# Optimization experiments

Hardware: AMD Instinct MI355X
Metric: run time of the kernel (lower is better)

Reference implementation:

```python
import jax, jax.numpy as jnp
import numpy as np

# dims
B, S, E, H, W = 32, 256, 512, 512, 512   # batch, max_sentence_length, word_emb, rnn_units, weight_size
ENC = 2 * H                               # bidirectional encoder hidden
V = 50000                                 # vocab


def setup_inputs() -> dict:
    key = jax.random.key(0)
    ks = jax.random.split(key, 16)
    n = jax.random.normal
    return {
        "word_ids": jax.random.randint(ks[0], (B, S), 0, V),
        "encoder_outputs": n(ks[1], (B, S, ENC), jnp.float32),
        "encoder_hn": n(ks[2], (B, H), jnp.float32),          # initial decoder cell state
        "emb": n(ks[3], (V, E), jnp.float32) * 0.02,          # WordFeature embedding table
        "chunk_emb": n(ks[4], (S, W), jnp.float32) * 0.02,    # chunk_length_embedding
        "W1": n(ks[5], (ENC, W), jnp.float32) / np.sqrt(ENC),
        "W2": n(ks[6], (E, W), jnp.float32) / np.sqrt(E),
        "W3": n(ks[7], (E, W), jnp.float32) / np.sqrt(E),
        "W4": n(ks[8], (H, W), jnp.float32) / np.sqrt(H),
        "vt1": n(ks[9], (W,), jnp.float32) / np.sqrt(W),
        "vt2": n(ks[10], (W,), jnp.float32) / np.sqrt(W),
        "Wx": n(ks[11], (E, 4 * H), jnp.float32) / np.sqrt(E),  # decoder LSTM cell
        "Wh": n(ks[12], (H, 4 * H), jnp.float32) / np.sqrt(H),
        "bias": jnp.zeros((4 * H,), jnp.float32),
    }


def reference(word_ids, encoder_outputs, encoder_hn, emb, chunk_emb,
              W1, W2, W3, W4, vt1, vt2, Wx, Wh, bias):
    Ss = word_ids.shape[1]
    Hh = encoder_hn.shape[1]
    inp = emb[word_ids]                                   # [B,S,E] word features
    b1 = jnp.einsum('bse,ew->bsw', encoder_outputs, W1)   # W1(encoder_output), hoisted
    b2 = jnp.einsum('bse,ew->bsw', inp, W2)               # W2(single_input), hoisted
    pos = jnp.arange(Ss)

    def decode_one(inp_b, b1_b, b2_b, c0):
        def step(carry, _):
            last_bond, bond, h, c, out_vec = carry
            done = bond >= Ss
            # decoder input: mean of current segment inp[last_bond:bond] (zeros at step 0)
            m = ((pos >= last_bond) & (pos < bond)).astype(inp_b.dtype)  # [S]
            x = (m @ inp_b) / jnp.maximum(m.sum(), 1.0)                  # [E]
            # LSTM cell (stand-in for decoder.pointer_forward)
            gates = x @ Wx + h @ Wh + bias                               # [4H]
            i_g, f_g, g_g, o_g = jnp.split(gates, 4)
            c_n = jax.nn.sigmoid(f_g) * c + jax.nn.sigmoid(i_g) * jnp.tanh(g_g)
            h_n = jax.nn.sigmoid(o_g) * jnp.tanh(c_n)
            h2 = jnp.where(done, h, h_n)
            c2 = jnp.where(done, c, c_n)
            bidx = jnp.minimum(bond, Ss - 1)
            # pointer attention over positions >= bond
            blend = jnp.tanh(b1_b + b2_b + inp_b[bidx] @ W3 + h2 @ W4)   # [S,W]
            seg_len = jnp.clip(bond - last_bond, 0, Ss - 1)
            scores = blend @ vt1 + chunk_emb[seg_len] @ vt2              # [S]
            scores = jnp.where(pos >= bidx, scores, -1e30)
            # log_softmax is monotonic -> argmax of scores == argmax of log-probs
            idx = jnp.argmax(scores)                                     # absolute = max_index + bond
            new_bond = jnp.where(idx > bond, idx, bond + 1)              # force progress
            widx = jnp.minimum(new_bond, Ss - 1)
            val = jnp.where((~done) & (new_bond < Ss), 1.0, out_vec[widx])
            out_new = out_vec.at[widx].set(val)
            last2 = jnp.where(done, last_bond, bond)
            bond2 = jnp.where(done, bond, new_bond)
            return (last2, bond2, h2, c2, out_new), None

        init = (jnp.int32(0), jnp.int32(0),
                jnp.zeros((Hh,), inp_b.dtype), c0,
                jnp.zeros((Ss,), inp_b.dtype))
        (_, _, _, _, out_vec), _ = jax.lax.scan(step, init, None, length=Ss)
        return out_vec

    outs = jax.vmap(decode_one)(inp, b1, b2, encoder_hn)   # [B,S]
    return outs.T                                          # [S,B] == torch.stack(output_list, 1)
```

## Files before the change

kernel.cpp:

```cpp
#include <hip/hip_runtime.h>
#include <math.h>

#define Bn   32
#define Sn   256
#define En   512
#define Hn   512
#define Wn   512
#define ENCn 1024
#define G4   2048
#define KTOT 1536

#define OFF_BSUM  0L
#define OFF_PWX   4194304L
#define OFF_PE    21037056L
#define OFF_U3    21037056L
#define OFF_WHB   25247744L
#define OFF_W4B   26296320L
#define OFF_GPH   26558464L
#define OFF_SPART 26689536L
#define OFF_STATE 26820608L

typedef unsigned long long u64t;

__device__ __forceinline__ float aload(const float* p) {
    return __hip_atomic_load(p, __ATOMIC_RELAXED, __HIP_MEMORY_SCOPE_AGENT);
}
__device__ __forceinline__ void astore(float* p, float v) {
    __hip_atomic_store(p, v, __ATOMIC_RELAXED, __HIP_MEMORY_SCOPE_AGENT);
}
__device__ __forceinline__ int aiload(const int* p) {
    return __hip_atomic_load(p, __ATOMIC_RELAXED, __HIP_MEMORY_SCOPE_AGENT);
}
__device__ __forceinline__ void aistore(int* p, int v) {
    __hip_atomic_store(p, v, __ATOMIC_RELAXED, __HIP_MEMORY_SCOPE_AGENT);
}
__device__ __forceinline__ u64t aload64(const u64t* p) {
    return __hip_atomic_load(p, __ATOMIC_RELAXED, __HIP_MEMORY_SCOPE_AGENT);
}
__device__ __forceinline__ void astore64(u64t* p, u64t v) {
    __hip_atomic_store(p, v, __ATOMIC_RELAXED, __HIP_MEMORY_SCOPE_AGENT);
}
__device__ __forceinline__ u64t pack2(float a, float b) {
    return (u64t)__float_as_uint(a) | ((u64t)__float_as_uint(b) << 32);
}
__device__ __forceinline__ float lo32(u64t v) { return __uint_as_float((unsigned)(v & 0xffffffffu)); }
__device__ __forceinline__ float hi32(u64t v) { return __uint_as_float((unsigned)(v >> 32)); }

__global__ void init_kernel(float* __restrict__ gph, int* __restrict__ state)
{
    int i = blockIdx.x * blockDim.x + threadIdx.x;
    if (i < 131072) gph[i] = 0.0f;
    if (i < 8192) state[i] = (i < 512) ? 1 : 0;
}

__global__ void wtrans_kernel(const float* __restrict__ Wh, const float* __restrict__ W4,
                              float* __restrict__ WhB, float* __restrict__ W4B)
{
    int idx = blockIdx.x * 256 + threadIdx.x;
    if (idx < 1048576) {
        const int c = idx & 255, k = (idx >> 8) & 511, cb = idx >> 17;
        WhB[idx] = Wh[(long)k * G4 + cb * 256 + c];
    }
    if (idx < 262144) {
        const int cc = idx & 3, l = (idx >> 2) & 63, kq = (idx >> 8) & 127, cb = idx >> 15;
        const int k = 4 * kq + cc, j = cb * 64 + l;
        W4B[idx] = W4[(long)k * Wn + j];
    }
}

__global__ void pe1_kernel(const int* __restrict__ wid, const float* __restrict__ emb,
                           float* __restrict__ pb)
{
    const int b = blockIdx.x, blk = blockIdx.y;
    __shared__ int wids[16];
    if (threadIdx.x < 16) wids[threadIdx.x] = wid[b * Sn + blk * 16 + threadIdx.x];
    __syncthreads();
    float a0 = 0.f, a1 = 0.f;
    for (int s = 0; s < 16; ++s) {
        const float* r = emb + (long)wids[s] * En;
        a0 += r[threadIdx.x]; a1 += r[threadIdx.x + 256];
    }
    pb[((long)b * 16 + blk) * En + threadIdx.x] = a0;
    pb[((long)b * 16 + blk) * En + threadIdx.x + 256] = a1;
}

__global__ void pe2_kernel(const int* __restrict__ wid, const float* __restrict__ emb,
                           const float* __restrict__ pb, float* __restrict__ pe)
{
    const int b = blockIdx.x, blk = blockIdx.y;
    __shared__ int wids[16];
    if (threadIdx.x < 16) wids[threadIdx.x] = wid[b * Sn + blk * 16 + threadIdx.x];
    __syncthreads();
    float a0 = 0.f, a1 = 0.f;
    for (int j = 0; j < blk; ++j) {
        a0 += pb[((long)b * 16 + j) * En + threadIdx.x];
        a1 += pb[((long)b * 16 + j) * En + threadIdx.x + 256];
    }
    float* base = pe + (long)b * 257 * En;
    if (blk == 0) { base[threadIdx.x] = 0.f; base[threadIdx.x + 256] = 0.f; }
    for (int s = 0; s < 16; ++s) {
        const float* r = emb + (long)wids[s] * En;
        a0 += r[threadIdx.x]; a1 += r[threadIdx.x + 256];
        float* o = base + (long)(blk * 16 + s + 1) * En;
        o[threadIdx.x] = a0; o[threadIdx.x + 256] = a1;
    }
}

__global__ __launch_bounds__(256) void bsum_gemm(
    const float* __restrict__ enc, const int* __restrict__ wid,
    const float* __restrict__ emb, const float* __restrict__ W1,
    const float* __restrict__ W2, float* __restrict__ bsum)
{
    __shared__ float As[16][68];
    __shared__ float Bs[16][68];
    const int tid  = threadIdx.x;
    const int row0 = blockIdx.y * 64;
    const int col0 = blockIdx.x * 64;
    const int tm0  = (tid & 15) * 4;
    const int tn0  = (tid >> 4) * 4;
    const int la_r = tid >> 2;
    const int la_k = (tid & 3) * 4;
    const int lb_k = tid >> 4;
    const int lb_n = (tid & 15) * 4;

    float acc[4][4];
#pragma unroll
    for (int i = 0; i < 4; i++)
#pragma unroll
        for (int j = 0; j < 4; j++) acc[i][j] = 0.0f;

    for (int k0 = 0; k0 < KTOT; k0 += 16) {
        const int gr = row0 + la_r;
        float4 av;
        if (k0 < ENCn) {
            av = *(const float4*)&enc[(long)gr * ENCn + k0 + la_k];
        } else {
            const int wv = wid[gr];
            av = *(const float4*)&emb[(long)wv * En + (k0 - ENCn) + la_k];
        }
        As[la_k + 0][la_r] = av.x;
        As[la_k + 1][la_r] = av.y;
        As[la_k + 2][la_r] = av.z;
        As[la_k + 3][la_r] = av.w;
        float4 bv;
        if (k0 < ENCn) bv = *(const float4*)&W1[(long)(k0 + lb_k) * Wn + col0 + lb_n];
        else           bv = *(const float4*)&W2[(long)(k0 - ENCn + lb_k) * Wn + col0 + lb_n];
        *(float4*)&Bs[lb_k][lb_n] = bv;
        __syncthreads();
#pragma unroll
        for (int kk = 0; kk < 16; kk++) {
            float4 a = *(const float4*)&As[kk][tm0];
            float4 b = *(const float4*)&Bs[kk][tn0];
            acc[0][0] += a.x * b.x; acc[0][1] += a.x * b.y; acc[0][2] += a.x * b.z; acc[0][3] += a.x * b.w;
            acc[1][0] += a.y * b.x; acc[1][1] += a.y * b.y; acc[1][2] += a.y * b.z; acc[1][3] += a.y * b.w;
            acc[2][0] += a.z * b.x; acc[2][1] += a.z * b.y; acc[2][2] += a.z * b.z; acc[2][3] += a.z * b.w;
            acc[3][0] += a.w * b.x; acc[3][1] += a.w * b.y; acc[3][2] += a.w * b.z; acc[3][3] += a.w * b.w;
        }
        __syncthreads();
    }
#pragma unroll
    for (int i = 0; i < 4; i++) {
        float4 o = make_float4(acc[i][0], acc[i][1], acc[i][2], acc[i][3]);
        *(float4*)&bsum[(long)(row0 + tm0 + i) * Wn + col0 + tn0] = o;
    }
}

__global__ __launch_bounds__(256) void swx_gemm(
    const float* __restrict__ pe, const float* __restrict__ Wx, float* __restrict__ PWX)
{
    __shared__ float As[16][68];
    __shared__ float Bs[16][68];
    const int tid  = threadIdx.x;
    const int row0 = blockIdx.y * 64;
    const int col0 = blockIdx.x * 64;
    const int tm0  = (tid & 15) * 4;
    const int tn0  = (tid >> 4) * 4;
    const int la_r = tid >> 2;
    const int la_k = (tid & 3) * 4;
    const int lb_k = tid >> 4;
    const int lb_n = (tid & 15) * 4;

    float acc[4][4];
#pragma unroll
    for (int i = 0; i < 4; i++)
#pragma unroll
        for (int j = 0; j < 4; j++) acc[i][j] = 0.0f;

    for (int k0 = 0; k0 < 512; k0 += 16) {
        int gr = row0 + la_r; if (gr > 8223) gr = 8223;
        float4 av = *(const float4*)&pe[(long)gr * En + k0 + la_k];
        As[la_k + 0][la_r] = av.x;
        As[la_k + 1][la_r] = av.y;
        As[la_k + 2][la_r] = av.z;
        As[la_k + 3][la_r] = av.w;
        *(float4*)&Bs[lb_k][lb_n] = *(const float4*)&Wx[(long)(k0 + lb_k) * G4 + col0 + lb_n];
        __syncthreads();
#pragma unroll
        for (int kk = 0; kk < 16; kk++) {
            float4 a = *(const float4*)&As[kk][tm0];
            float4 b = *(const float4*)&Bs[kk][tn0];
            acc[0][0] += a.x * b.x; acc[0][1] += a.x * b.y; acc[0][2] += a.x * b.z; acc[0][3] += a.x * b.w;
            acc[1][0] += a.y * b.x; acc[1][1] += a.y * b.y; acc[1][2] += a.y * b.z; acc[1][3] += a.y * b.w;
            acc[2][0] += a.z * b.x; acc[2][1] += a.z * b.y; acc[2][2] += a.z * b.z; acc[2][3] += a.z * b.w;
            acc[3][0] += a.w * b.x; acc[3][1] += a.w * b.y; acc[3][2] += a.w * b.z; acc[3][3] += a.w * b.w;
        }
        __syncthreads();
    }
#pragma unroll
    for (int i = 0; i < 4; i++) {
        const int r = row0 + tm0 + i;
        if (r < 8224) {
            float4 o = make_float4(acc[i][0], acc[i][1], acc[i][2], acc[i][3]);
            *(float4*)&PWX[(long)r * G4 + col0 + tn0] = o;
        }
    }
}

__global__ __launch_bounds__(256) void u3_gemm(
    const int* __restrict__ wid, const float* __restrict__ emb,
    const float* __restrict__ W3, float* __restrict__ u3)
{
    __shared__ float As[16][68];
    __shared__ float Bs[16][68];
    const int tid  = threadIdx.x;
    const int row0 = blockIdx.y * 64;
    const int col0 = blockIdx.x * 64;
    const int tm0  = (tid & 15) * 4;
    const int tn0  = (tid >> 4) * 4;
    const int la_r = tid >> 2;
    const int la_k = (tid & 3) * 4;
    const int lb_k = tid >> 4;
    const int lb_n = (tid & 15) * 4;

    float acc[4][4];
#pragma unroll
    for (int i = 0; i < 4; i++)
#pragma unroll
        for (int j = 0; j < 4; j++) acc[i][j] = 0.0f;

    for (int k0 = 0; k0 < 512; k0 += 16) {
        const int gr = row0 + la_r;
        const int wv = wid[gr];
        float4 av = *(const float4*)&emb[(long)wv * En + k0 + la_k];
        As[la_k + 0][la_r] = av.x;
        As[la_k + 1][la_r] = av.y;
        As[la_k + 2][la_r] = av.z;
        As[la_k + 3][la_r] = av.w;
        *(float4*)&Bs[lb_k][lb_n] = *(const float4*)&W3[(long)(k0 + lb_k) * Wn + col0 + lb_n];
        __syncthreads();
#pragma unroll
        for (int kk = 0; kk < 16; kk++) {
            float4 a = *(const float4*)&As[kk][tm0];
            float4 b = *(const float4*)&Bs[kk][tn0];
            acc[0][0] += a.x * b.x; acc[0][1] += a.x * b.y; acc[0][2] += a.x * b.z; acc[0][3] += a.x * b.w;
            acc[1][0] += a.y * b.x; acc[1][1] += a.y * b.y; acc[1][2] += a.y * b.z; acc[1][3] += a.y * b.w;
            acc[2][0] += a.z * b.x; acc[2][1] += a.z * b.y; acc[2][2] += a.z * b.z; acc[2][3] += a.z * b.w;
            acc[3][0] += a.w * b.x; acc[3][1] += a.w * b.y; acc[3][2] += a.w * b.z; acc[3][3] += a.w * b.w;
        }
        __syncthreads();
    }
#pragma unroll
    for (int i = 0; i < 4; i++) {
        float4 o = make_float4(acc[i][0], acc[i][1], acc[i][2], acc[i][3]);
        *(float4*)&u3[(long)(row0 + tm0 + i) * Wn + col0 + tn0] = o;
    }
}

__global__ __launch_bounds__(256) void decode_kernel(
    const float* __restrict__ bias, const float* __restrict__ vt1,
    const float* __restrict__ bsum, const float* __restrict__ u3,
    const float* __restrict__ PWX,  const float* __restrict__ WhB,
    const float* __restrict__ W4B,  float* __restrict__ gphbuf,
    float* __restrict__ spart, int* __restrict__ state,
    const float* __restrict__ hn0, float* __restrict__ out)
{
    __shared__ __align__(16) float wlds[32768];
    __shared__ __align__(16) float pwx[2][2048];
    __shared__ __align__(16) float hld[512];
    __shared__ __align__(16) float cld[512];
    __shared__ __align__(16) float sgph[4][256];
    __shared__ __align__(16) float sred4[4][64];
    __shared__ float qv[64];
    __shared__ float s_svt[64];
    __shared__ float s_wv[4];
    __shared__ int   s_wi[4];

    const int wg   = blockIdx.x;
    const int tid  = threadIdx.x;
    const int lane = tid & 63;
    const int wv   = tid >> 6;
    const int b    = wg >> 3;
    const int cb2  = wg & 7;

    int* gflag = state;
    int* sflag = state + 512;
    u64t* gph64 = (u64t*)gphbuf;
    const float4* W4B4 = (const float4*)W4B;
    float4* wlds4 = (float4*)wlds;
    const float4* h4 = (const float4*)hld;

    {
        const float4* src = W4B4 + (long)cb2 * 8192;
        for (int i = tid; i < 8192; i += 256) wlds4[i] = src[i];
    }
    if (tid < 64) s_svt[tid] = vt1[cb2 * 64 + tid];
    cld[tid]       = hn0[b * Hn + tid];
    cld[256 + tid] = hn0[b * Hn + 256 + tid];
    hld[tid] = 0.f; hld[256 + tid] = 0.f;
    {
        const float4* pr = (const float4*)(PWX + (long)b * 257 * G4);
        float4* d = (float4*)pwx[0];
        for (int i = tid; i < 512; i += 256) d[i] = pr[i];
    }
    const float2* bias2 = (const float2*)bias;
    const float2 bi  = bias2[tid];
    const float2 bf  = bias2[256 + tid];
    const float2 bg_ = bias2[512 + tid];
    const float2 bo  = bias2[768 + tid];
    __syncthreads();

    int bd = 0, ls = 0;

    for (int t = 1; t <= Sn; ++t) {
        const int cur = t & 1, prv = cur ^ 1;

        if (tid < 8) {
            const int* g = gflag + 16 * b + tid;
            while (aiload(g) < t) __builtin_amdgcn_s_sleep(1);
        }
        __syncthreads();
        {
            const float4* pr = (const float4*)(PWX + ((long)b * 257 + bd) * G4);
            float4* d = (float4*)pwx[cur];
            for (int i = tid; i < 512; i += 256) d[i] = pr[i];
        }
        float u3v = 0.f;
        if (tid < 64) u3v = aload(&u3[((long)b * Sn + bd) * Wn + cb2 * 64 + tid]);
        const long gb = (long)cur * 32768 + (long)b * 1024;
        const u64t g0 = aload64(&gph64[gb + tid]);
        const u64t g1 = aload64(&gph64[gb + 256 + tid]);
        const u64t g2 = aload64(&gph64[gb + 512 + tid]);
        const u64t g3 = aload64(&gph64[gb + 768 + tid]);
        __syncthreads();

        {
            const float inv = 1.0f / (float)max(bd - ls, 1);
            const int j0 = 2 * tid, j1 = j0 + 1;
            const float igA = (pwx[cur][j0]        - pwx[prv][j0])        * inv + lo32(g0) + bi.x;
            const float igB = (pwx[cur][j1]        - pwx[prv][j1])        * inv + hi32(g0) + bi.y;
            const float fgA = (pwx[cur][512 + j0]  - pwx[prv][512 + j0])  * inv + lo32(g1) + bf.x;
            const float fgB = (pwx[cur][512 + j1]  - pwx[prv][512 + j1])  * inv + hi32(g1) + bf.y;
            const float ggA = (pwx[cur][1024 + j0] - pwx[prv][1024 + j0]) * inv + lo32(g2) + bg_.x;
            const float ggB = (pwx[cur][1024 + j1] - pwx[prv][1024 + j1]) * inv + hi32(g2) + bg_.y;
            const float ogA = (pwx[cur][1536 + j0] - pwx[prv][1536 + j0]) * inv + lo32(g3) + bo.x;
            const float ogB = (pwx[cur][1536 + j1] - pwx[prv][1536 + j1]) * inv + hi32(g3) + bo.y;
            const float sfA = 1.f / (1.f + expf(-fgA));
            const float siA = 1.f / (1.f + expf(-igA));
            const float soA = 1.f / (1.f + expf(-ogA));
            const float cnA = sfA * cld[j0] + siA * tanhf(ggA);
            const float h2A = soA * tanhf(cnA);
            const float sfB = 1.f / (1.f + expf(-fgB));
            const float siB = 1.f / (1.f + expf(-igB));
            const float soB = 1.f / (1.f + expf(-ogB));
            const float cnB = sfB * cld[j1] + siB * tanhf(ggB);
            const float h2B = soB * tanhf(cnB);
            cld[j0] = cnA; hld[j0] = h2A;
            cld[j1] = cnB; hld[j1] = h2B;
        }
        __syncthreads();

        {
            float acc = 0.f;
            const float4* wr = wlds4 + (wv * 32) * 64 + lane;
#pragma unroll 8
            for (int kq = 0; kq < 32; ++kq) {
                const float4 w = wr[kq * 64];
                const float4 hv = h4[wv * 32 + kq];
                acc += w.x * hv.x + w.y * hv.y + w.z * hv.z + w.w * hv.w;
            }
            sred4[wv][lane] = acc;
        }
        __syncthreads();
        if (tid < 64) qv[tid] = sred4[0][tid] + sred4[1][tid] + sred4[2][tid] + sred4[3][tid] + u3v;
        __syncthreads();

        if (tid >= bd) {
            const float* row = bsum + ((long)b * Sn + tid) * Wn + cb2 * 64;
            float a = 0.f;
#pragma unroll 8
            for (int i = 0; i < 64; ++i)
                a += tanhf(row[i] + qv[i]) * s_svt[i];
            astore(&spart[(long)cur * 65536 + (long)b * 2048 + cb2 * 256 + tid], a);
        }

        {
            float4 acc = make_float4(0.f, 0.f, 0.f, 0.f);
            const float* wb = WhB + (long)cb2 * 131072;
            const int k0 = wv * 128;
#pragma unroll 4
            for (int k = k0; k < k0 + 128; ++k) {
                const float hk = hld[k];
                const float4 w = *(const float4*)&wb[(long)k * 256 + lane * 4];
                acc.x += hk * w.x; acc.y += hk * w.y; acc.z += hk * w.z; acc.w += hk * w.w;
            }
            *(float4*)&sgph[wv][lane * 4] = acc;
        }
        __syncthreads();
        if (tid < 128) {
            const int c0 = 2 * tid, c1 = c0 + 1;
            const float lo = sgph[0][c0] + sgph[1][c0] + sgph[2][c0] + sgph[3][c0];
            const float hi = sgph[0][c1] + sgph[1][c1] + sgph[2][c1] + sgph[3][c1];
            astore64(&gph64[(long)prv * 32768 + (long)b * 1024 + cb2 * 128 + tid], pack2(lo, hi));
        }
        __syncthreads();

        if (tid == 0) {
            aistore(&sflag[16 * b + cb2], t);
            aistore(&gflag[16 * b + cb2], t + 1);
        }
        if (tid < 8) {
            const int* s = sflag + 16 * b + tid;
            while (aiload(s) < t) __builtin_amdgcn_s_sleep(1);
        }
        __syncthreads();
        float v = -3.402823e38f; int vi = Sn;
        if (tid >= bd) {
            const float* sp = spart + (long)cur * 65536 + (long)b * 2048 + tid;
            float s = 0.f;
#pragma unroll
            for (int k = 0; k < 8; ++k) s += aload(&sp[k * 256]);
            v = s; vi = tid;
        }
#pragma unroll
        for (int off = 32; off; off >>= 1) {
            const float v2 = __shfl_xor(v, off, 64);
            const int   i2 = __shfl_xor(vi, off, 64);
            if (v2 > v || (v2 == v && i2 < vi)) { v = v2; vi = i2; }
        }
        if (lane == 0) { s_wv[wv] = v; s_wi[wv] = vi; }
        __syncthreads();
        {
            float bv = s_wv[0]; int bi_ = s_wi[0];
#pragma unroll
            for (int k = 1; k < 4; ++k)
                if (s_wv[k] > bv || (s_wv[k] == bv && s_wi[k] < bi_)) { bv = s_wv[k]; bi_ = s_wi[k]; }
            const int nb = (bi_ > bd) ? bi_ : bd + 1;
            if (cb2 == 0 && tid == 0 && nb < Sn) out[nb * Bn + b] = 1.0f;
            ls = bd; bd = nb;
        }
        __syncthreads();
        if (bd >= Sn) break;
    }
}

extern "C" void kernel_launch(void* const* d_in, const int* in_sizes, int n_in,
                              void* d_out, int out_size, void* d_ws, size_t ws_size,
                              hipStream_t stream)
{
    const int*   wid  = (const int*)d_in[0];
    const float* enc  = (const float*)d_in[1];
    const float* hn0  = (const float*)d_in[2];
    const float* emb  = (const float*)d_in[3];
    const float* W1   = (const float*)d_in[5];
    const float* W2   = (const float*)d_in[6];
    const float* W3   = (const float*)d_in[7];
    const float* W4   = (const float*)d_in[8];
    const float* vt1  = (const float*)d_in[9];
    const float* Wx   = (const float*)d_in[11];
    const float* Wh   = (const float*)d_in[12];
    const float* bias = (const float*)d_in[13];

    float* ws    = (float*)d_ws;
    float* bsum  = ws + OFF_BSUM;
    float* PWX   = ws + OFF_PWX;
    float* pe    = ws + OFF_PE;
    float* pb    = ws + OFF_WHB;
    float* u3    = ws + OFF_U3;
    float* WhB   = ws + OFF_WHB;
    float* W4B   = ws + OFF_W4B;
    float* gph   = ws + OFF_GPH;
    float* spart = ws + OFF_SPART;
    int*   state = (int*)(ws + OFF_STATE);
    float* out   = (float*)d_out;

    pb = ws + OFF_BSUM;

    (void)hipMemsetAsync(d_out, 0, (size_t)Sn * Bn * sizeof(float), stream);
    hipLaunchKernelGGL(init_kernel, dim3(544), dim3(256), 0, stream, gph, state);
    hipLaunchKernelGGL(wtrans_kernel, dim3(4096), dim3(256), 0, stream, Wh, W4, WhB, W4B);
    hipLaunchKernelGGL(pe1_kernel, dim3(32, 16), dim3(256), 0, stream, wid, emb, pb);
    hipLaunchKernelGGL(pe2_kernel, dim3(32, 16), dim3(256), 0, stream, wid, emb, pb, pe);
    hipLaunchKernelGGL(swx_gemm, dim3(32, 129), dim3(256), 0, stream, pe, Wx, PWX);
    hipLaunchKernelGGL(u3_gemm, dim3(8, 128), dim3(256), 0, stream, wid, emb, W3, u3);
    hipLaunchKernelGGL(bsum_gemm, dim3(8, 128), dim3(256), 0, stream, enc, wid, emb, W1, W2, bsum);

    void* args[] = { (void*)&bias, (void*)&vt1, (void*)&bsum, (void*)&u3, (void*)&PWX,
                     (void*)&WhB, (void*)&W4B, (void*)&gph, (void*)&spart,
                     (void*)&state, (void*)&hn0, (void*)&out };
    (void)hipLaunchCooperativeKernel((void*)decode_kernel, dim3(256), dim3(256), args, 0, stream);
}
```

Baseline: 940.7 us.

## Compute per-step x@Wx in decode loop and replace score flag barrier with tagged values

The large precomputed prefix-sum GEMM (pe @ Wx for every position) is removed. Instead, each decode step forms the segment-mean input vector from prefix sums and multiplies it by a blocked copy of Wx inside the cooperative kernel, exchanging partial gate sums through a new double-buffered global array. The score partials are now stored as 64-bit value+step-tag pairs, so readers spin on the tag instead of a separate sflag barrier. The next step's gate computation is moved after the argmax. This trades a big upfront GEMM and its memory traffic for extra per-step serial work of about 512x2048 per batch row on the critical path.

```diff
diff --git a/kernel.cpp b/kernel.cpp
--- a/kernel.cpp
+++ b/kernel.cpp
@@ -11,14 +11,15 @@
 #define KTOT 1536
 
 #define OFF_BSUM  0L
-#define OFF_PWX   4194304L
-#define OFF_PE    21037056L
-#define OFF_U3    21037056L
-#define OFF_WHB   25247744L
-#define OFF_W4B   26296320L
-#define OFF_GPH   26558464L
-#define OFF_SPART 26689536L
-#define OFF_STATE 26820608L
+#define OFF_U3    4194304L
+#define OFF_PE    8388608L
+#define OFF_WXB   12599296L
+#define OFF_WHB   13647872L
+#define OFF_W4B   14696448L
+#define OFF_GXW   14958592L
+#define OFF_GPH   15089664L
+#define OFF_SPART 15220736L
+#define OFF_STATE 15482880L
 
 typedef unsigned long long u64t;
 
@@ -43,22 +44,29 @@
 __device__ __forceinline__ u64t pack2(float a, float b) {
     return (u64t)__float_as_uint(a) | ((u64t)__float_as_uint(b) << 32);
 }
+__device__ __forceinline__ u64t packtag(float a, int t) {
+    return (u64t)__float_as_uint(a) | ((u64t)(unsigned)t << 32);
+}
 __device__ __forceinline__ float lo32(u64t v) { return __uint_as_float((unsigned)(v & 0xffffffffu)); }
 __device__ __forceinline__ float hi32(u64t v) { return __uint_as_float((unsigned)(v >> 32)); }
 
-__global__ void init_kernel(float* __restrict__ gph, int* __restrict__ state)
+__global__ void init_kernel(float* __restrict__ gxw, float* __restrict__ gph,
+                            float* __restrict__ sp2, int* __restrict__ state)
 {
     int i = blockIdx.x * blockDim.x + threadIdx.x;
-    if (i < 131072) gph[i] = 0.0f;
+    if (i < 131072) { gxw[i] = 0.0f; gph[i] = 0.0f; }
+    if (i < 262144) sp2[i] = 0.0f;
     if (i < 8192) state[i] = (i < 512) ? 1 : 0;
 }
 
-__global__ void wtrans_kernel(const float* __restrict__ Wh, const float* __restrict__ W4,
+__global__ void wtrans_kernel(const float* __restrict__ Wx, const float* __restrict__ Wh,
+                              const float* __restrict__ W4, float* __restrict__ WxB,
                               float* __restrict__ WhB, float* __restrict__ W4B)
 {
     int idx = blockIdx.x * 256 + threadIdx.x;
     if (idx < 1048576) {
         const int c = idx & 255, k = (idx >> 8) & 511, cb = idx >> 17;
+        WxB[idx] = Wx[(long)k * G4 + cb * 256 + c];
         WhB[idx] = Wh[(long)k * G4 + cb * 256 + c];
     }
     if (idx < 262144) {
@@ -165,8 +173,9 @@
     }
 }
 
-__global__ __launch_bounds__(256) void swx_gemm(
-    const float* __restrict__ pe, const float* __restrict__ Wx, float* __restrict__ PWX)
+__global__ __launch_bounds__(256) void u3_gemm(
+    const int* __restrict__ wid, const float* __restrict__ emb,
+    const float* __restrict__ W3, float* __restrict__ u3)
 {
     __shared__ float As[16][68];
     __shared__ float Bs[16][68];
@@ -187,58 +196,6 @@
         for (int j = 0; j < 4; j++) acc[i][j] = 0.0f;
 
     for (int k0 = 0; k0 < 512; k0 += 16) {
-        int gr = row0 + la_r; if (gr > 8223) gr = 8223;
-        float4 av = *(const float4*)&pe[(long)gr * En + k0 + la_k];
-        As[la_k + 0][la_r] = av.x;
-        As[la_k + 1][la_r] = av.y;
-        As[la_k + 2][la_r] = av.z;
-        As[la_k + 3][la_r] = av.w;
-        *(float4*)&Bs[lb_k][lb_n] = *(const float4*)&Wx[(long)(k0 + lb_k) * G4 + col0 + lb_n];
-        __syncthreads();
-#pragma unroll
-        for (int kk = 0; kk < 16; kk++) {
-            float4 a = *(const float4*)&As[kk][tm0];
-            float4 b = *(const float4*)&Bs[kk][tn0];
-            acc[0][0] += a.x * b.x; acc[0][1] += a.x * b.y; acc[0][2] += a.x * b.z; acc[0][3] += a.x * b.w;
-            acc[1][0] += a.y * b.x; acc[1][1] += a.y * b.y; acc[1][2] += a.y * b.z; acc[1][3] += a.y * b.w;
-            acc[2][0] += a.z * b.x; acc[2][1] += a.z * b.y; acc[2][2] += a.z * b.z; acc[2][3] += a.z * b.w;
-            acc[3][0] += a.w * b.x; acc[3][1] += a.w * b.y; acc[3][2] += a.w * b.z; acc[3][3] += a.w * b.w;
-        }
-        __syncthreads();
-    }
-#pragma unroll
-    for (int i = 0; i < 4; i++) {
-        const int r = row0 + tm0 + i;
-        if (r < 8224) {
-            float4 o = make_float4(acc[i][0], acc[i][1], acc[i][2], acc[i][3]);
-            *(float4*)&PWX[(long)r * G4 + col0 + tn0] = o;
-        }
-    }
-}
-
-__global__ __launch_bounds__(256) void u3_gemm(
-    const int* __restrict__ wid, const float* __restrict__ emb,
-    const float* __restrict__ W3, float* __restrict__ u3)
-{
-    __shared__ float As[16][68];
-    __shared__ float Bs[16][68];
-    const int tid  = threadIdx.x;
-    const int row0 = blockIdx.y * 64;
-    const int col0 = blockIdx.x * 64;
-    const int tm0  = (tid & 15) * 4;
-    const int tn0  = (tid >> 4) * 4;
-    const int la_r = tid >> 2;
-    const int la_k = (tid & 3) * 4;
-    const int lb_k = tid >> 4;
-    const int lb_n = (tid & 15) * 4;
-
-    float acc[4][4];
-#pragma unroll
-    for (int i = 0; i < 4; i++)
-#pragma unroll
-        for (int j = 0; j < 4; j++) acc[i][j] = 0.0f;
-
-    for (int k0 = 0; k0 < 512; k0 += 16) {
         const int gr = row0 + la_r;
         const int wv = wid[gr];
         float4 av = *(const float4*)&emb[(long)wv * En + k0 + la_k];
@@ -269,16 +226,17 @@
 __global__ __launch_bounds__(256) void decode_kernel(
     const float* __restrict__ bias, const float* __restrict__ vt1,
     const float* __restrict__ bsum, const float* __restrict__ u3,
-    const float* __restrict__ PWX,  const float* __restrict__ WhB,
-    const float* __restrict__ W4B,  float* __restrict__ gphbuf,
-    float* __restrict__ spart, int* __restrict__ state,
+    const float* __restrict__ pe,   const float* __restrict__ WxB,
+    const float* __restrict__ WhB,  const float* __restrict__ W4B,
+    float* __restrict__ gxwbuf, float* __restrict__ gphbuf,
+    u64t* __restrict__ spart2, int* __restrict__ state,
     const float* __restrict__ hn0, float* __restrict__ out)
 {
     __shared__ __align__(16) float wlds[32768];
-    __shared__ __align__(16) float pwx[2][2048];
     __shared__ __align__(16) float hld[512];
     __shared__ __align__(16) float cld[512];
-    __shared__ __align__(16) float sgph[4][256];
+    __shared__ __align__(16) float xld[512];
+    __shared__ __align__(16) float sgp[4][256];
     __shared__ __align__(16) float sred4[4][64];
     __shared__ float qv[64];
     __shared__ float s_svt[64];
@@ -293,11 +251,12 @@
     const int cb2  = wg & 7;
 
     int* gflag = state;
-    int* sflag = state + 512;
+    u64t* gxw64 = (u64t*)gxwbuf;
     u64t* gph64 = (u64t*)gphbuf;
     const float4* W4B4 = (const float4*)W4B;
     float4* wlds4 = (float4*)wlds;
     const float4* h4 = (const float4*)hld;
+    const float2* pef2 = (const float2*)pe;
 
     {
         const float4* src = W4B4 + (long)cb2 * 8192;
@@ -307,11 +266,6 @@
     cld[tid]       = hn0[b * Hn + tid];
     cld[256 + tid] = hn0[b * Hn + 256 + tid];
     hld[tid] = 0.f; hld[256 + tid] = 0.f;
-    {
-        const float4* pr = (const float4*)(PWX + (long)b * 257 * G4);
-        float4* d = (float4*)pwx[0];
-        for (int i = tid; i < 512; i += 256) d[i] = pr[i];
-    }
     const float2* bias2 = (const float2*)bias;
     const float2 bi  = bias2[tid];
     const float2 bf  = bias2[256 + tid];
@@ -322,38 +276,36 @@
     int bd = 0, ls = 0;
 
     for (int t = 1; t <= Sn; ++t) {
-        const int cur = t & 1, prv = cur ^ 1;
+        const long cur = (long)(t & 1) * 32768;
+        const long scur = (long)(t & 1) * 65536;
 
         if (tid < 8) {
             const int* g = gflag + 16 * b + tid;
             while (aiload(g) < t) __builtin_amdgcn_s_sleep(1);
         }
         __syncthreads();
-        {
-            const float4* pr = (const float4*)(PWX + ((long)b * 257 + bd) * G4);
-            float4* d = (float4*)pwx[cur];
-            for (int i = tid; i < 512; i += 256) d[i] = pr[i];
-        }
         float u3v = 0.f;
         if (tid < 64) u3v = aload(&u3[((long)b * Sn + bd) * Wn + cb2 * 64 + tid]);
-        const long gb = (long)cur * 32768 + (long)b * 1024;
-        const u64t g0 = aload64(&gph64[gb + tid]);
-        const u64t g1 = aload64(&gph64[gb + 256 + tid]);
-        const u64t g2 = aload64(&gph64[gb + 512 + tid]);
-        const u64t g3 = aload64(&gph64[gb + 768 + tid]);
-        __syncthreads();
-
-        {
-            const float inv = 1.0f / (float)max(bd - ls, 1);
+        const long gb = cur + (long)b * 1024;
+        const u64t gx0 = aload64(&gxw64[gb + tid]);
+        const u64t gx1 = aload64(&gxw64[gb + 256 + tid]);
+        const u64t gx2 = aload64(&gxw64[gb + 512 + tid]);
+        const u64t gx3 = aload64(&gxw64[gb + 768 + tid]);
+        const u64t gh0 = aload64(&gph64[gb + tid]);
+        const u64t gh1 = aload64(&gph64[gb + 256 + tid]);
+        const u64t gh2 = aload64(&gph64[gb + 512 + tid]);
+        const u64t gh3 = aload64(&gph64[gb + 768 + tid]);
+
+        {
             const int j0 = 2 * tid, j1 = j0 + 1;
-            const float igA = (pwx[cur][j0]        - pwx[prv][j0])        * inv + lo32(g0) + bi.x;
-            const float igB = (pwx[cur][j1]        - pwx[prv][j1])        * inv + hi32(g0) + bi.y;
-            const float fgA = (pwx[cur][512 + j0]  - pwx[prv][512 + j0])  * inv + lo32(g1) + bf.x;
-            const float fgB = (pwx[cur][512 + j1]  - pwx[prv][512 + j1])  * inv + hi32(g1) + bf.y;
-            const float ggA = (pwx[cur][1024 + j0] - pwx[prv][1024 + j0]) * inv + lo32(g2) + bg_.x;
-            const float ggB = (pwx[cur][1024 + j1] - pwx[prv][1024 + j1]) * inv + hi32(g2) + bg_.y;
-            const float ogA = (pwx[cur][1536 + j0] - pwx[prv][1536 + j0]) * inv + lo32(g3) + bo.x;
-            const float ogB = (pwx[cur][1536 + j1] - pwx[prv][1536 + j1]) * inv + hi32(g3) + bo.y;
+            const float igA = lo32(gx0) + lo32(gh0) + bi.x;
+            const float igB = hi32(gx0) + hi32(gh0) + bi.y;
+            const float fgA = lo32(gx1) + lo32(gh1) + bf.x;
+            const float fgB = hi32(gx1) + hi32(gh1) + bf.y;
+            const float ggA = lo32(gx2) + lo32(gh2) + bg_.x;
+            const float ggB = hi32(gx2) + hi32(gh2) + bg_.y;
+            const float ogA = lo32(gx3) + lo32(gh3) + bo.x;
+            const float ogB = hi32(gx3) + hi32(gh3) + bo.y;
             const float sfA = 1.f / (1.f + expf(-fgA));
             const float siA = 1.f / (1.f + expf(-igA));
             const float soA = 1.f / (1.f + expf(-ogA));
@@ -390,9 +342,52 @@
 #pragma unroll 8
             for (int i = 0; i < 64; ++i)
                 a += tanhf(row[i] + qv[i]) * s_svt[i];
-            astore(&spart[(long)cur * 65536 + (long)b * 2048 + cb2 * 256 + tid], a);
-        }
-
+            astore64(&spart2[scur + (long)b * 2048 + cb2 * 256 + tid], packtag(a, t));
+        }
+
+        float v = -3.402823e38f; int vi = Sn;
+        if (tid >= bd) {
+            const u64t* sp = spart2 + scur + (long)b * 2048 + tid;
+            u64t e0, e1, e2, e3, e4, e5, e6, e7;
+            for (;;) {
+                e0 = aload64(&sp[0]);    e1 = aload64(&sp[256]);
+                e2 = aload64(&sp[512]);  e3 = aload64(&sp[768]);
+                e4 = aload64(&sp[1024]); e5 = aload64(&sp[1280]);
+                e6 = aload64(&sp[1536]); e7 = aload64(&sp[1792]);
+                const unsigned tt = (unsigned)t;
+                if ((unsigned)(e0 >> 32) == tt && (unsigned)(e1 >> 32) == tt &&
+                    (unsigned)(e2 >> 32) == tt && (unsigned)(e3 >> 32) == tt &&
+                    (unsigned)(e4 >> 32) == tt && (unsigned)(e5 >> 32) == tt &&
+                    (unsigned)(e6 >> 32) == tt && (unsigned)(e7 >> 32) == tt) break;
+                __builtin_amdgcn_s_sleep(1);
+            }
+            v = lo32(e0) + lo32(e1) + lo32(e2) + lo32(e3)
+              + lo32(e4) + lo32(e5) + lo32(e6) + lo32(e7);
+            vi = tid;
+        }
+#pragma unroll
+        for (int off = 32; off; off >>= 1) {
+            const float v2 = __shfl_xor(v, off, 64);
+            const int   i2 = __shfl_xor(vi, off, 64);
+            if (v2 > v || (v2 == v && i2 < vi)) { v = v2; vi = i2; }
+        }
+        if (lane == 0) { s_wv[wv] = v; s_wi[wv] = vi; }
+        __syncthreads();
+        {
+            float bv = s_wv[0]; int bi_ = s_wi[0];
+#pragma unroll
+            for (int k = 1; k < 4; ++k)
+                if (s_wv[k] > bv || (s_wv[k] == bv && s_wi[k] < bi_)) { bv = s_wv[k]; bi_ = s_wi[k]; }
+            const int nb = (bi_ > bd) ? bi_ : bd + 1;
+            if (cb2 == 0 && tid == 0 && nb < Sn) out[nb * Bn + b] = 1.0f;
+            ls = bd; bd = nb;
+        }
+        __syncthreads();
+        if (bd >= Sn) break;
+
+        const long nxt = (long)((t + 1) & 1) * 32768;
+        const float2 pa  = pef2[((long)b * 257 + bd) * 256 + tid];
+        const float2 pb_ = pef2[((long)b * 257 + ls) * 256 + tid];
         {
             float4 acc = make_float4(0.f, 0.f, 0.f, 0.f);
             const float* wb = WhB + (long)cb2 * 131072;
@@ -403,53 +398,42 @@
                 const float4 w = *(const float4*)&wb[(long)k * 256 + lane * 4];
                 acc.x += hk * w.x; acc.y += hk * w.y; acc.z += hk * w.z; acc.w += hk * w.w;
             }
-            *(float4*)&sgph[wv][lane * 4] = acc;
+            *(float4*)&sgp[wv][lane * 4] = acc;
+        }
+        {
+            const float inv = 1.0f / (float)max(bd - ls, 1);
+            xld[2 * tid]     = (pa.x - pb_.x) * inv;
+            xld[2 * tid + 1] = (pa.y - pb_.y) * inv;
         }
         __syncthreads();
         if (tid < 128) {
             const int c0 = 2 * tid, c1 = c0 + 1;
-            const float lo = sgph[0][c0] + sgph[1][c0] + sgph[2][c0] + sgph[3][c0];
-            const float hi = sgph[0][c1] + sgph[1][c1] + sgph[2][c1] + sgph[3][c1];
-            astore64(&gph64[(long)prv * 32768 + (long)b * 1024 + cb2 * 128 + tid], pack2(lo, hi));
-        }
-        __syncthreads();
-
-        if (tid == 0) {
-            aistore(&sflag[16 * b + cb2], t);
-            aistore(&gflag[16 * b + cb2], t + 1);
-        }
-        if (tid < 8) {
-            const int* s = sflag + 16 * b + tid;
-            while (aiload(s) < t) __builtin_amdgcn_s_sleep(1);
-        }
-        __syncthreads();
-        float v = -3.402823e38f; int vi = Sn;
-        if (tid >= bd) {
-            const float* sp = spart + (long)cur * 65536 + (long)b * 2048 + tid;
-            float s = 0.f;
-#pragma unroll
-            for (int k = 0; k < 8; ++k) s += aload(&sp[k * 256]);
-            v = s; vi = tid;
-        }
-#pragma unroll
-        for (int off = 32; off; off >>= 1) {
-            const float v2 = __shfl_xor(v, off, 64);
-            const int   i2 = __shfl_xor(vi, off, 64);
-            if (v2 > v || (v2 == v && i2 < vi)) { v = v2; vi = i2; }
-        }
-        if (lane == 0) { s_wv[wv] = v; s_wi[wv] = vi; }
-        __syncthreads();
-        {
-            float bv = s_wv[0]; int bi_ = s_wi[0];
-#pragma unroll
-            for (int k = 1; k < 4; ++k)
-                if (s_wv[k] > bv || (s_wv[k] == bv && s_wi[k] < bi_)) { bv = s_wv[k]; bi_ = s_wi[k]; }
-            const int nb = (bi_ > bd) ? bi_ : bd + 1;
-            if (cb2 == 0 && tid == 0 && nb < Sn) out[nb * Bn + b] = 1.0f;
-            ls = bd; bd = nb;
-        }
-        __syncthreads();
-        if (bd >= Sn) break;
+            const float lo = sgp[0][c0] + sgp[1][c0] + sgp[2][c0] + sgp[3][c0];
+            const float hi = sgp[0][c1] + sgp[1][c1] + sgp[2][c1] + sgp[3][c1];
+            astore64(&gph64[nxt + (long)b * 1024 + cb2 * 128 + tid], pack2(lo, hi));
+        }
+        __syncthreads();
+        {
+            float4 acc = make_float4(0.f, 0.f, 0.f, 0.f);
+            const float* wb = WxB + (long)cb2 * 131072;
+            const int k0 = wv * 128;
+#pragma unroll 4
+            for (int k = k0; k < k0 + 128; ++k) {
+                const float xk = xld[k];
+                const float4 w = *(const float4*)&wb[(long)k * 256 + lane * 4];
+                acc.x += xk * w.x; acc.y += xk * w.y; acc.z += xk * w.z; acc.w += xk * w.w;
+            }
+            *(float4*)&sgp[wv][lane * 4] = acc;
+        }
+        __syncthreads();
+        if (tid < 128) {
+            const int c0 = 2 * tid, c1 = c0 + 1;
+            const float lo = sgp[0][c0] + sgp[1][c0] + sgp[2][c0] + sgp[3][c0];
+            const float hi = sgp[0][c1] + sgp[1][c1] + sgp[2][c1] + sgp[3][c1];
+            astore64(&gxw64[nxt + (long)b * 1024 + cb2 * 128 + tid], pack2(lo, hi));
+        }
+        __syncthreads();
+        if (tid == 0) aistore(&gflag[16 * b + cb2], t + 1);
     }
 }
 
@@ -472,30 +456,29 @@
 
     float* ws    = (float*)d_ws;
     float* bsum  = ws + OFF_BSUM;
-    float* PWX   = ws + OFF_PWX;
+    float* u3    = ws + OFF_U3;
     float* pe    = ws + OFF_PE;
-    float* pb    = ws + OFF_WHB;
-    float* u3    = ws + OFF_U3;
+    float* WxB   = ws + OFF_WXB;
     float* WhB   = ws + OFF_WHB;
     float* W4B   = ws + OFF_W4B;
+    float* gxw   = ws + OFF_GXW;
     float* gph   = ws + OFF_GPH;
-    float* spart = ws + OFF_SPART;
+    float* sp2f  = ws + OFF_SPART;
+    u64t*  sp2   = (u64t*)sp2f;
     int*   state = (int*)(ws + OFF_STATE);
     float* out   = (float*)d_out;
-
-    pb = ws + OFF_BSUM;
+    float* pb    = ws + OFF_BSUM;
 
     (void)hipMemsetAsync(d_out, 0, (size_t)Sn * Bn * sizeof(float), stream);
-    hipLaunchKernelGGL(init_kernel, dim3(544), dim3(256), 0, stream, gph, state);
-    hipLaunchKernelGGL(wtrans_kernel, dim3(4096), dim3(256), 0, stream, Wh, W4, WhB, W4B);
+    hipLaunchKernelGGL(init_kernel, dim3(1024), dim3(256), 0, stream, gxw, gph, sp2f, state);
+    hipLaunchKernelGGL(wtrans_kernel, dim3(4096), dim3(256), 0, stream, Wx, Wh, W4, WxB, WhB, W4B);
     hipLaunchKernelGGL(pe1_kernel, dim3(32, 16), dim3(256), 0, stream, wid, emb, pb);
     hipLaunchKernelGGL(pe2_kernel, dim3(32, 16), dim3(256), 0, stream, wid, emb, pb, pe);
-    hipLaunchKernelGGL(swx_gemm, dim3(32, 129), dim3(256), 0, stream, pe, Wx, PWX);
     hipLaunchKernelGGL(u3_gemm, dim3(8, 128), dim3(256), 0, stream, wid, emb, W3, u3);
     hipLaunchKernelGGL(bsum_gemm, dim3(8, 128), dim3(256), 0, stream, enc, wid, emb, W1, W2, bsum);
 
-    void* args[] = { (void*)&bias, (void*)&vt1, (void*)&bsum, (void*)&u3, (void*)&PWX,
-                     (void*)&WhB, (void*)&W4B, (void*)&gph, (void*)&spart,
-                     (void*)&state, (void*)&hn0, (void*)&out };
+    void* args[] = { (void*)&bias, (void*)&vt1, (void*)&bsum, (void*)&u3, (void*)&pe,
+                     (void*)&WxB, (void*)&WhB, (void*)&W4B, (void*)&gxw, (void*)&gph,
+                     (void*)&sp2, (void*)&state, (void*)&hn0, (void*)&out };
     (void)hipLaunchCooperativeKernel((void*)decode_kernel, dim3(256), dim3(256), args, 0, stream);
 }
```

New measurement: 787.4 us. 16.3% less time.
